# Kernel optimization log

Measured on AMD Instinct MI355X. Metric: run time of the kernel, lower is better.

## Reference

```python
import jax, jax.numpy as jnp
import numpy as np

B, L, C = 8, 2048, 512
CI = C // 2  # internal_units


def setup_inputs() -> dict:
    key = jax.random.key(0)
    ks = jax.random.split(key, 4)
    inputs = jax.random.normal(ks[0], (B, L, C), dtype=jnp.float32)
    # Conv1D kernel_size=1 == per-position linear; kernel_initializer='random_normal' (stddev 0.05)
    Wx = 0.05 * jax.random.normal(ks[1], (C, CI), dtype=jnp.float32)
    Wy = 0.05 * jax.random.normal(ks[2], (C, CI), dtype=jnp.float32)
    Wo = 0.05 * jax.random.normal(ks[3], (C, C), dtype=jnp.float32)
    bx = jnp.zeros((CI,), dtype=jnp.float32)
    by = jnp.zeros((CI,), dtype=jnp.float32)
    bo = jnp.zeros((C,), dtype=jnp.float32)
    return {"inputs": inputs, "Wx": Wx, "bx": bx, "Wy": Wy, "by": by, "Wo": Wo, "bo": bo}


def reference(inputs, Wx, bx, Wy, by, Wo, bo):
    # 1x1 conv projections (per-position linear layers with bias)
    x_proj = jnp.einsum('blc,ci->bli', inputs, Wx) + bx   # [B, L, Ci]
    y_proj = jnp.einsum('blc,ci->bli', inputs, Wy) + by   # [B, L, Ci]
    o_proj = jnp.einsum('blc,cd->bld', inputs, Wo) + bo   # [B, L, C]
    # scores: batched matmul x @ y^T -> [B, L, L]
    scores = jnp.einsum('bli,bmi->blm', x_proj, y_proj)
    # NOTE: softmax over axis=0 (the BATCH axis), as in the original module
    attn = jax.nn.softmax(scores, axis=0)
    s_dot = jnp.einsum('blm,bmc->blc', attn, o_proj)       # [B, L, C]
    return inputs + s_dot
```

## Files before the change

kernel.cpp:

```cpp
#include <hip/hip_runtime.h>


#define NB 8
#define NL 2048
#define NC 512
#define NCI 256

using f16x8 = __attribute__((ext_vector_type(8))) _Float16;
using f32x4 = __attribute__((ext_vector_type(4))) float;
typedef unsigned short u16;

__device__ __forceinline__ u16 f16b(float x) {
    _Float16 h = (_Float16)x;
    return __builtin_bit_cast(u16, h);
}
__device__ __forceinline__ float f16tof(u16 u) {
    return (float)__builtin_bit_cast(_Float16, u);
}
__device__ __forceinline__ void gload16(const void* g, void* l) {
    __builtin_amdgcn_global_load_lds((__attribute__((address_space(1))) void*)g,
                                     (__attribute__((address_space(3))) void*)l,
                                     16, 0, 0);
}

__global__ __launch_bounds__(256) void cvt_x_kernel(const float* __restrict__ X,
                                                    u16* __restrict__ Xf)
{
    size_t i = (size_t)blockIdx.x * 256 + threadIdx.x;
    const float4* X4 = (const float4*)X;
    float4 a = X4[2 * i], b = X4[2 * i + 1];
    u16 o[8] = {f16b(a.x), f16b(a.y), f16b(a.z), f16b(a.w),
                f16b(b.x), f16b(b.y), f16b(b.z), f16b(b.w)};
    ((uint4*)Xf)[i] = *(const uint4*)o;
}

__global__ __launch_bounds__(256) void cvt_w_kernel(
    const float* __restrict__ Wx, const float* __restrict__ Wy, const float* __restrict__ Wo,
    u16* __restrict__ WxT, u16* __restrict__ WyT, u16* __restrict__ WoT)
{
    const int bid = blockIdx.x, t = threadIdx.x;
#pragma unroll
    for (int kk = 0; kk < 2; ++kk) {
        const int k = t + kk * 256;
        if (bid < 256)      WxT[(size_t)bid * NC + k] = f16b(Wx[(size_t)k * NCI + bid]);
        else if (bid < 512) WyT[(size_t)(bid - 256) * NC + k] = f16b(Wy[(size_t)k * NCI + (bid - 256)]);
        else                WoT[(size_t)(bid - 512) * NC + k] = f16b(Wo[(size_t)k * NC + (bid - 512)]);
    }
}

__global__ __launch_bounds__(256) void proj_kernel(
    const u16* __restrict__ Xf,
    const u16* __restrict__ WxT, const u16* __restrict__ WyT, const u16* __restrict__ WoT,
    const float* __restrict__ bx, const float* __restrict__ by, const float* __restrict__ bo,
    u16* __restrict__ xp, u16* __restrict__ yp, u16* __restrict__ opT)
{
    __shared__ __align__(16) u16 SM[17408];
    u16* As = SM;
    u16* Bs = SM + 8192;

    const int tid = threadIdx.x;
    const int w = tid >> 6, lane = tid & 63;
    const int row0 = blockIdx.x * 128;
    const int cb = blockIdx.y;

    const u16* W; const float* bias; int n0, path;
    if (cb < 2)      { path = 0; n0 = cb * 128;       W = WxT; bias = bx; }
    else if (cb < 4) { path = 1; n0 = (cb - 2) * 128; W = WyT; bias = by; }
    else             { path = 2; n0 = (cb - 4) * 128; W = WoT; bias = bo; }

    f32x4 acc[4][4] = {};
    const int wm = (w & 1) * 64, wn = (w >> 1) * 64;
    const int fr = lane & 15, fq = lane >> 4;

    for (int k0 = 0; k0 < NC; k0 += 64) {
#pragma unroll
        for (int pass = 0; pass < 4; ++pass) {
            const int cbase = pass * 256 + w * 64;
            const int chunk = cbase + lane;
            const int r = chunk >> 3;
            const int kc = (chunk & 7) ^ (r & 7);
            gload16(Xf + (size_t)(row0 + r) * NC + k0 + kc * 8, (char*)As + cbase * 16);
            gload16(W  + (size_t)(n0  + r) * NC + k0 + kc * 8, (char*)Bs + cbase * 16);
        }
        __syncthreads();
        f16x8 a[4][2], b[4][2];
#pragma unroll
        for (int mi = 0; mi < 4; ++mi)
#pragma unroll
            for (int kt = 0; kt < 2; ++kt)
                a[mi][kt] = *(const f16x8*)&As[(wm + mi * 16 + fr) * 64 + ((kt * 4 + fq) ^ (fr & 7)) * 8];
#pragma unroll
        for (int ni = 0; ni < 4; ++ni)
#pragma unroll
            for (int kt = 0; kt < 2; ++kt)
                b[ni][kt] = *(const f16x8*)&Bs[(wn + ni * 16 + fr) * 64 + ((kt * 4 + fq) ^ (fr & 7)) * 8];
#pragma unroll
        for (int kt = 0; kt < 2; ++kt)
#pragma unroll
            for (int mi = 0; mi < 4; ++mi)
#pragma unroll
                for (int ni = 0; ni < 4; ++ni)
                    acc[mi][ni] = __builtin_amdgcn_mfma_f32_16x16x32_f16(a[mi][kt], b[ni][kt], acc[mi][ni], 0, 0, 0);
        __syncthreads();
    }

    if (path != 2) {
        u16* O = (path == 0) ? xp : yp;
#pragma unroll
        for (int mi = 0; mi < 4; ++mi) {
            const int grow = row0 + wm + mi * 16 + fq * 4;
#pragma unroll
            for (int ni = 0; ni < 4; ++ni) {
                const int gcol = n0 + wn + ni * 16 + fr;
                const float bv = bias[gcol];
#pragma unroll
                for (int r = 0; r < 4; ++r)
                    O[(size_t)(grow + r) * NCI + gcol] = f16b(acc[mi][ni][r] + bv);
            }
        }
    } else {
        u16* Ts = SM;
#pragma unroll
        for (int mi = 0; mi < 4; ++mi) {
            const int mb = wm + mi * 16 + fq * 4;
#pragma unroll
            for (int ni = 0; ni < 4; ++ni) {
                const int nl_ = wn + ni * 16 + fr;
                const float bv = bias[n0 + nl_];
#pragma unroll
                for (int r = 0; r < 4; ++r)
                    Ts[nl_ * 136 + mb + r] = f16b(acc[mi][ni][r] + bv);
            }
        }
        __syncthreads();
        const int b = row0 >> 11, m0 = row0 & 2047;
        u16* dst = opT + (size_t)b * NC * NL + (size_t)n0 * NL + m0;
        for (int i = tid; i < 128 * 16; i += 256) {
            const int c = i >> 4, ch = i & 15;
            uint4 v = *(const uint4*)&Ts[c * 136 + ch * 8];
            *(uint4*)&dst[(size_t)c * NL + ch * 8] = v;
        }
    }
}

__global__ __launch_bounds__(512, 4) void score_softmax_kernel(
    const u16* __restrict__ xp, const u16* __restrict__ yp, u16* __restrict__ ATT)
{
    __shared__ __align__(16) u16 SM[33280];
    const int tid = threadIdx.x;
    const int w = tid >> 6, lane = tid & 63;
    const int row0 = blockIdx.x * 64, col0 = blockIdx.y * 64;
    const int bb = w & 3, nh = w >> 2;
    const int fr = lane & 15, fq = lane >> 4;

    const int rs = (tid >> 3) & 63;
    const int jj = (tid & 7) ^ (rs & 7);

    unsigned sv[2][16];

#pragma unroll
    for (int g = 0; g < 2; ++g) {
        f32x4 acc[4][2] = {};
#pragma unroll
        for (int s = 0; s < 4; ++s) {
            const int k0 = s * 64;
#pragma unroll
            for (int pass = 0; pass < 8; ++pass) {
                const int ab = pass >> 2, b2 = pass & 3;
                const u16* src = (ab ? yp : xp)
                    + (size_t)(g * 4 + b2) * NL * NCI
                    + (size_t)((ab ? col0 : row0) + rs) * NCI + k0 + jj * 8;
                gload16(src, (char*)SM + pass * 8192 + tid * 16);
            }
            __syncthreads();
#pragma unroll
            for (int kt = 0; kt < 2; ++kt) {
                const int coff = ((kt * 4 + fq) ^ (fr & 7)) * 8;
                f16x8 af[4], bf[2];
#pragma unroll
                for (int mi = 0; mi < 4; ++mi)
                    af[mi] = *(const f16x8*)&SM[bb * 4096 + (mi * 16 + fr) * 64 + coff];
#pragma unroll
                for (int ni = 0; ni < 2; ++ni)
                    bf[ni] = *(const f16x8*)&SM[16384 + bb * 4096 + (nh * 32 + ni * 16 + fr) * 64 + coff];
#pragma unroll
                for (int mi = 0; mi < 4; ++mi)
#pragma unroll
                    for (int ni = 0; ni < 2; ++ni)
                        acc[mi][ni] = __builtin_amdgcn_mfma_f32_16x16x32_f16(af[mi], bf[ni], acc[mi][ni], 0, 0, 0);
            }
            __syncthreads();
        }
#pragma unroll
        for (int mi = 0; mi < 4; ++mi)
#pragma unroll
            for (int ni = 0; ni < 2; ++ni) {
                sv[g][mi * 4 + ni * 2 + 0] = (unsigned)f16b(acc[mi][ni][0]) | ((unsigned)f16b(acc[mi][ni][1]) << 16);
                sv[g][mi * 4 + ni * 2 + 1] = (unsigned)f16b(acc[mi][ni][2]) | ((unsigned)f16b(acc[mi][ni][3]) << 16);
            }
    }

#pragma unroll
    for (int g = 0; g < 2; ++g)
#pragma unroll
        for (int mi = 0; mi < 4; ++mi)
#pragma unroll
            for (int ni = 0; ni < 2; ++ni)
#pragma unroll
                for (int rp = 0; rp < 2; ++rp) {
                    const unsigned u = sv[g][mi * 4 + ni * 2 + rp];
                    const int r_ = mi * 16 + fq * 4 + rp * 2;
                    const int c_ = nh * 32 + ni * 16 + fr;
                    SM[(r_ * 65 + c_) * 8 + g * 4 + bb]         = (u16)(u & 0xFFFF);
                    SM[((r_ + 1) * 65 + c_) * 8 + g * 4 + bb]   = (u16)(u >> 16);
                }
    __syncthreads();

#pragma unroll
    for (int j = 0; j < 8; ++j) {
        const int row = j * 8 + w;
        const int col = lane;
        const uint4 v = *(const uint4*)&SM[(row * 65 + col) * 8];
        float f[NB];
        f[0] = f16tof((u16)(v.x & 0xFFFF)); f[1] = f16tof((u16)(v.x >> 16));
        f[2] = f16tof((u16)(v.y & 0xFFFF)); f[3] = f16tof((u16)(v.y >> 16));
        f[4] = f16tof((u16)(v.z & 0xFFFF)); f[5] = f16tof((u16)(v.z >> 16));
        f[6] = f16tof((u16)(v.w & 0xFFFF)); f[7] = f16tof((u16)(v.w >> 16));
        float m = f[0];
#pragma unroll
        for (int b = 1; b < NB; ++b) m = fmaxf(m, f[b]);
        float ssum = 0.f;
#pragma unroll
        for (int b = 0; b < NB; ++b) { f[b] = __expf(f[b] - m); ssum += f[b]; }
        const float inv = 1.f / ssum;
        const size_t go = (size_t)(row0 + row) * NL + col0 + col;
#pragma unroll
        for (int b = 0; b < NB; ++b)
            ATT[(size_t)b * NL * NL + go] = f16b(f[b] * inv);
    }
}

__global__ __launch_bounds__(512) void out_kernel(
    const u16* __restrict__ ATT, const u16* __restrict__ opT,
    const float* __restrict__ X, float* __restrict__ Out)
{
    __shared__ __align__(16) u16 As[2][8192], Bs[2][8192];
    const int tid = threadIdx.x;
    const int w = tid >> 6, lane = tid & 63;

    const int id  = blockIdx.x + 16 * (blockIdx.y + 4 * blockIdx.z);
    const int nid = (id & 7) * 64 + (id >> 3);
    const int bx  = nid & 15;
    const int by  = (nid >> 4) & 3;
    const int b   = nid >> 6;

    const int row0 = bx * 128, col0 = by * 128;
    const u16* Aatt = ATT + (size_t)b * NL * NL;
    const u16* Bsrc = opT + (size_t)b * NC * NL;

    f32x4 acc[4][2] = {};
    const int wm = (w & 1) * 64, wn = (w >> 1) * 32;
    const int fr = lane & 15, fq = lane >> 4;

    auto stage = [&](int k0, int bu) {
#pragma unroll
        for (int pass = 0; pass < 2; ++pass) {
            const int cbase = pass * 512 + w * 64;
            const int chunk = cbase + lane;
            const int r = chunk >> 3;
            const int kc = (chunk & 7) ^ (r & 7);
            gload16(Aatt + (size_t)(row0 + r) * NL + k0 + kc * 8, (char*)&As[bu][0] + cbase * 16);
            gload16(Bsrc + (size_t)(col0 + r) * NL + k0 + kc * 8, (char*)&Bs[bu][0] + cbase * 16);
        }
    };

    stage(0, 0);
    int bu = 0;
    for (int it = 0; it < NL / 64; ++it) {
        __syncthreads();
        if (it + 1 < NL / 64) stage((it + 1) * 64, bu ^ 1);
        f16x8 af[4][2], bf[2][2];
#pragma unroll
        for (int mi = 0; mi < 4; ++mi)
#pragma unroll
            for (int kt = 0; kt < 2; ++kt)
                af[mi][kt] = *(const f16x8*)&As[bu][(wm + mi * 16 + fr) * 64 + ((kt * 4 + fq) ^ (fr & 7)) * 8];
#pragma unroll
        for (int ni = 0; ni < 2; ++ni)
#pragma unroll
            for (int kt = 0; kt < 2; ++kt)
                bf[ni][kt] = *(const f16x8*)&Bs[bu][(wn + ni * 16 + fr) * 64 + ((kt * 4 + fq) ^ (fr & 7)) * 8];
#pragma unroll
        for (int kt = 0; kt < 2; ++kt)
#pragma unroll
            for (int mi = 0; mi < 4; ++mi)
#pragma unroll
                for (int ni = 0; ni < 2; ++ni)
                    acc[mi][ni] = __builtin_amdgcn_mfma_f32_16x16x32_f16(af[mi][kt], bf[ni][kt], acc[mi][ni], 0, 0, 0);
        bu ^= 1;
    }
    const size_t ob = (size_t)b * NL * NC;
#pragma unroll
    for (int mi = 0; mi < 4; ++mi) {
        const int gr = row0 + wm + mi * 16 + fq * 4;
#pragma unroll
        for (int ni = 0; ni < 2; ++ni) {
            const int gc = col0 + wn + ni * 16 + fr;
#pragma unroll
            for (int r = 0; r < 4; ++r) {
                const size_t o = ob + (size_t)(gr + r) * NC + gc;
                Out[o] = X[o] + acc[mi][ni][r];
            }
        }
    }
}

extern "C" void kernel_launch(void* const* d_in, const int* in_sizes, int n_in,
                              void* d_out, int out_size, void* d_ws, size_t ws_size,
                              hipStream_t stream)
{
    const float* X  = (const float*)d_in[0];
    const float* Wx = (const float*)d_in[1];
    const float* bx = (const float*)d_in[2];
    const float* Wy = (const float*)d_in[3];
    const float* by = (const float*)d_in[4];
    const float* Wo = (const float*)d_in[5];
    const float* bo = (const float*)d_in[6];
    float* out = (float*)d_out;

    char* ws = (char*)d_ws;
    u16* ATT = (u16*)ws;
    u16* Xf  = (u16*)ws;
    char* p = ws + 67108864;
    u16* xp  = (u16*)p; p += 8388608;
    u16* yp  = (u16*)p; p += 8388608;
    u16* opT = (u16*)p; p += 16777216;
    u16* WxT = (u16*)p; p += 262144;
    u16* WyT = (u16*)p; p += 262144;
    u16* WoT = (u16*)p; p += 524288;

    cvt_x_kernel<<<4096, 256, 0, stream>>>(X, Xf);
    cvt_w_kernel<<<1024, 256, 0, stream>>>(Wx, Wy, Wo, WxT, WyT, WoT);
    proj_kernel<<<dim3(128, 8), 256, 0, stream>>>(Xf, WxT, WyT, WoT, bx, by, bo, xp, yp, opT);
    score_softmax_kernel<<<dim3(32, 32), 512, 0, stream>>>(xp, yp, ATT);
    out_kernel<<<dim3(16, 4, NB), 512, 0, stream>>>(ATT, opT, X, out);
}
```

Before: 208.2 us.

## Replace double-buffered K=64 staging with single-buffered K=128 tiles in out_kernel

The attention-times-values GEMM in out_kernel drops its two-stage LDS ping-pong with 64-wide K steps. Each iteration now loads a 128-wide K slab into one buffer, synchronises, computes, and synchronises again. This halves the number of loop iterations and barrier pairs per K, at the cost of losing the overlap between global loads and MFMA compute within a block.

```diff
diff --git a/kernel.cpp b/kernel.cpp
--- a/kernel.cpp
+++ b/kernel.cpp
@@ -244,7 +244,7 @@
     const u16* __restrict__ ATT, const u16* __restrict__ opT,
     const float* __restrict__ X, float* __restrict__ Out)
 {
-    __shared__ __align__(16) u16 As[2][8192], Bs[2][8192];
+    __shared__ __align__(16) u16 As[16384], Bs[16384];
     const int tid = threadIdx.x;
     const int w = tid >> 6, lane = tid & 63;
 
@@ -262,42 +262,39 @@
     const int wm = (w & 1) * 64, wn = (w >> 1) * 32;
     const int fr = lane & 15, fq = lane >> 4;
 
-    auto stage = [&](int k0, int bu) {
-#pragma unroll
-        for (int pass = 0; pass < 2; ++pass) {
-            const int cbase = pass * 512 + w * 64;
-            const int chunk = cbase + lane;
-            const int r = chunk >> 3;
-            const int kc = (chunk & 7) ^ (r & 7);
-            gload16(Aatt + (size_t)(row0 + r) * NL + k0 + kc * 8, (char*)&As[bu][0] + cbase * 16);
-            gload16(Bsrc + (size_t)(col0 + r) * NL + k0 + kc * 8, (char*)&Bs[bu][0] + cbase * 16);
-        }
-    };
-
-    stage(0, 0);
-    int bu = 0;
-    for (int it = 0; it < NL / 64; ++it) {
-        __syncthreads();
-        if (it + 1 < NL / 64) stage((it + 1) * 64, bu ^ 1);
-        f16x8 af[4][2], bf[2][2];
-#pragma unroll
-        for (int mi = 0; mi < 4; ++mi)
-#pragma unroll
-            for (int kt = 0; kt < 2; ++kt)
-                af[mi][kt] = *(const f16x8*)&As[bu][(wm + mi * 16 + fr) * 64 + ((kt * 4 + fq) ^ (fr & 7)) * 8];
-#pragma unroll
-        for (int ni = 0; ni < 2; ++ni)
-#pragma unroll
-            for (int kt = 0; kt < 2; ++kt)
-                bf[ni][kt] = *(const f16x8*)&Bs[bu][(wn + ni * 16 + fr) * 64 + ((kt * 4 + fq) ^ (fr & 7)) * 8];
-#pragma unroll
-        for (int kt = 0; kt < 2; ++kt)
-#pragma unroll
-            for (int mi = 0; mi < 4; ++mi)
+    for (int it = 0; it < NL / 128; ++it) {
+        const int k0 = it * 128;
+#pragma unroll
+        for (int pass = 0; pass < 4; ++pass) {
+            const int c = pass * 512 + tid;
+            const int kh = c >> 10;
+            const int r = (c >> 3) & 127;
+            const int jj = (c & 7) ^ (r & 7);
+            const int srck = k0 + kh * 64 + jj * 8;
+            gload16(Aatt + (size_t)(row0 + r) * NL + srck, (char*)As + c * 16);
+            gload16(Bsrc + (size_t)(col0 + r) * NL + srck, (char*)Bs + c * 16);
+        }
+        __syncthreads();
+#pragma unroll
+        for (int kh = 0; kh < 2; ++kh)
+#pragma unroll
+            for (int kt = 0; kt < 2; ++kt) {
+                const int hb = kh * 8192;
+                const int coff = ((kt * 4 + fq) ^ (fr & 7)) * 8;
+                f16x8 af[4], bf[2];
+#pragma unroll
+                for (int mi = 0; mi < 4; ++mi)
+                    af[mi] = *(const f16x8*)&As[hb + (wm + mi * 16 + fr) * 64 + coff];
 #pragma unroll
                 for (int ni = 0; ni < 2; ++ni)
-                    acc[mi][ni] = __builtin_amdgcn_mfma_f32_16x16x32_f16(af[mi][kt], bf[ni][kt], acc[mi][ni], 0, 0, 0);
-        bu ^= 1;
+                    bf[ni] = *(const f16x8*)&Bs[hb + (wn + ni * 16 + fr) * 64 + coff];
+#pragma unroll
+                for (int mi = 0; mi < 4; ++mi)
+#pragma unroll
+                    for (int ni = 0; ni < 2; ++ni)
+                        acc[mi][ni] = __builtin_amdgcn_mfma_f32_16x16x32_f16(af[mi], bf[ni], acc[mi][ni], 0, 0, 0);
+            }
+        __syncthreads();
     }
     const size_t ob = (size_t)b * NL * NC;
 #pragma unroll
```

After: 200.9 us. 1.04x faster.
